# Kernel optimization log

Hardware: AMD Instinct MI355X
Metric: run time of the kernel (lower is better)

Reference implementation:

```python
import jax, jax.numpy as jnp
import numpy as np

B, C, H, W = 8, 512, 64, 64
R = 16
CQK = C // R  # 32


def setup_inputs() -> dict:
    key = jax.random.key(0)
    kx, kq, kk, kv = jax.random.split(key, 4)
    x = jax.random.normal(kx, (B, C, H, W), dtype=jnp.float32)
    # Conv1d with kernel_size=1, bias=False == matmul over channel dim
    Wq = jax.random.normal(kq, (CQK, C), dtype=jnp.float32) * (1.0 / np.sqrt(C))
    Wk = jax.random.normal(kk, (CQK, C), dtype=jnp.float32) * (1.0 / np.sqrt(C))
    Wv = jax.random.normal(kv, (C, C), dtype=jnp.float32) * (1.0 / np.sqrt(C))
    return {"x": x, "Wq": Wq, "Wk": Wk, "Wv": Wv}


def reference(x, Wq, Wk, Wv):
    b, c, h, w = x.shape
    xf = x.reshape(b, c, h * w)                 # [b, c, n]
    q = jnp.einsum('dc,bcn->bdn', Wq, xf)       # [b, c/r, n]
    k = jnp.einsum('dc,bcn->bdn', Wk, xf)       # [b, c/r, n]
    attn = jax.nn.softmax(jnp.einsum('bdm,bdn->bmn', q, k), axis=-1)  # [b, n, n]
    v = jnp.einsum('dc,bcn->bdn', Wv, xf)       # [b, c, n]
    out = jnp.einsum('bcm,bmn->bcn', v, attn)   # [b, c, n]
    return out.reshape(b, c, h, w)
```

## Files before the change

### kernel.cpp

```cpp
#include <hip/hip_runtime.h>
#include <hip/hip_bf16.h>


typedef __attribute__((ext_vector_type(8))) short s16x8;
typedef __attribute__((ext_vector_type(4))) float f32x4;

#define MFMA16(a, b, c) __builtin_amdgcn_mfma_f32_16x16x32_bf16((a), (b), (c), 0, 0, 0)

__device__ __forceinline__ ushort f2bf(float f) {
  union { float f; unsigned u; } v; v.f = f;
  return (ushort)((v.u + 0x8000u) >> 16);
}
__device__ __forceinline__ unsigned pack_bf16(float lo, float hi) {
  union { float f; unsigned u; } a, b; a.f = lo; b.f = hi;
  return __builtin_amdgcn_perm(b.u + 0x8000u, a.u + 0x8000u, 0x07060302u);
}
__device__ __forceinline__ float fexp2(float x) { return __builtin_amdgcn_exp2f(x); }

__device__ __forceinline__ void chunk_barrier() {
  asm volatile("s_waitcnt lgkmcnt(0)" ::: "memory");
  __builtin_amdgcn_s_barrier();
  __builtin_amdgcn_sched_barrier(0);
}

__global__ void k_cvt_w(const float* __restrict__ Wq, const float* __restrict__ Wk,
                        const float* __restrict__ Wv, ushort* __restrict__ Wqb,
                        ushort* __restrict__ Wkb, ushort* __restrict__ Wvb) {
  int i = blockIdx.x * 256 + threadIdx.x;
  if (i < 262144) Wvb[i] = f2bf(Wv[i]);
  else if (i < 278528) Wqb[i - 262144] = f2bf(Wq[i - 262144] * 1.4426950408889634f);
  else if (i < 294912) Wkb[i - 278528] = f2bf(Wk[i - 278528]);
}

__global__ __launch_bounds__(256, 2) void k_proj(const float* __restrict__ x,
                                                 const ushort* __restrict__ Wqb,
                                                 const ushort* __restrict__ Wkb,
                                                 const ushort* __restrict__ Wvb,
                                                 ushort* __restrict__ qb,
                                                 ushort* __restrict__ kb,
                                                 ushort* __restrict__ vb) {
  const int b = blockIdx.y, n0 = blockIdx.x * 64;
  const int t = threadIdx.x;
  const int lane = t & 63, w = t >> 6;
  const int quad = lane >> 4, l15 = lane & 15;

  __shared__ __align__(16) ushort XB[64 * 512];
  __shared__ uint U[2][32][17];

  const float* x_b = x + (size_t)b * 512 * 4096;

  for (int s = 0; s < 16; ++s) {
    const int c0s = s * 32;
#pragma unroll
    for (int k = 0; k < 2; ++k) {
      const int idx = t + k * 256;
      const int cr = idx >> 4, c4 = idx & 15;
      float4 f = *(const float4*)(x_b + (size_t)(c0s + cr) * 4096 + n0 + c4 * 4);
      U[0][cr][c4] = pack_bf16(f.x, f.y);
      U[1][cr][c4] = pack_bf16(f.z, f.w);
    }
    __syncthreads();
    {
      const int n = t & 63, gl = t >> 6;
      const int h = (n >> 1) & 1, c4 = n >> 2;
      const uint sel = (n & 1) ? 0x07060302u : 0x05040100u;
      uint o[4];
#pragma unroll
      for (int j = 0; j < 4; ++j) {
        uint ua = U[h][gl * 8 + 2 * j][c4];
        uint ub = U[h][gl * 8 + 2 * j + 1][c4];
        o[j] = __builtin_amdgcn_perm(ub, ua, sel);
      }
      const int gfull = (c0s >> 3) + gl;
      const int gsw = gfull ^ (n & 7);
      *(uint4*)((char*)XB + n * 1024 + gsw * 16) = *(uint4*)o;
    }
    __syncthreads();
  }

  const ushort* Wqk = (w < 2) ? (Wqb + (size_t)(w * 16 + l15) * 512)
                              : (Wkb + (size_t)((w - 2) * 16 + l15) * 512);

  f32x4 accv[8][4], accqk[4];
#pragma unroll
  for (int i = 0; i < 8; ++i)
#pragma unroll
    for (int nt = 0; nt < 4; ++nt) accv[i][nt] = {0.f, 0.f, 0.f, 0.f};
#pragma unroll
  for (int nt = 0; nt < 4; ++nt) accqk[nt] = {0.f, 0.f, 0.f, 0.f};

  const char* XBb = (const char*)XB;
  for (int k0 = 0; k0 < 512; k0 += 32) {
    s16x8 bx[4];
#pragma unroll
    for (int nt = 0; nt < 4; ++nt) {
      const int nl = nt * 16 + l15;
      bx[nt] = *(const s16x8*)(XBb + nl * 1024 + ((((k0 >> 3) + quad) ^ (nl & 7)) << 4));
    }
#pragma unroll
    for (int i = 0; i < 8; ++i) {
      s16x8 av = *(const s16x8*)(Wvb + (size_t)((8 * w + i) * 16 + l15) * 512 + k0 + quad * 8);
#pragma unroll
      for (int nt = 0; nt < 4; ++nt) accv[i][nt] = MFMA16(av, bx[nt], accv[i][nt]);
    }
    s16x8 aqk = *(const s16x8*)(Wqk + k0 + quad * 8);
#pragma unroll
    for (int nt = 0; nt < 4; ++nt) accqk[nt] = MFMA16(aqk, bx[nt], accqk[nt]);
  }

  ushort* vb_b = vb + (size_t)b * 512 * 4096;
#pragma unroll
  for (int i = 0; i < 8; ++i)
#pragma unroll
    for (int nt = 0; nt < 4; ++nt)
#pragma unroll
      for (int r = 0; r < 4; ++r)
        vb_b[(size_t)((8 * w + i) * 16 + quad * 4 + r) * 4096 + n0 + nt * 16 + l15] =
            f2bf(accv[i][nt][r]);

  ushort* qk_out = (w < 2) ? (qb + (size_t)b * 4096 * 32) : (kb + (size_t)b * 4096 * 32);
#pragma unroll
  for (int nt = 0; nt < 4; ++nt) {
    ushort4 u;
    u.x = f2bf(accqk[nt][0]); u.y = f2bf(accqk[nt][1]);
    u.z = f2bf(accqk[nt][2]); u.w = f2bf(accqk[nt][3]);
    *(ushort4*)(qk_out + (size_t)(n0 + nt * 16 + l15) * 32 + (w & 1) * 16 + quad * 4) = u;
  }
}

__global__ __launch_bounds__(256) void k_pass1(const ushort* __restrict__ qb,
                                               const ushort* __restrict__ kb,
                                               float* __restrict__ Lneg) {
  const int b = blockIdx.y, mt = blockIdx.x;
  const int lane = threadIdx.x & 63, w = threadIdx.x >> 6;
  const int quad = lane >> 4, l15 = lane & 15;
  const int m = mt * 64 + w * 16;
  const ushort* qb_b = qb + (size_t)b * 4096 * 32;
  const ushort* kb_b = kb + (size_t)b * 4096 * 32;
  const s16x8 aqf = *(const s16x8*)(qb_b + (size_t)(m + l15) * 32 + quad * 8);
  float ps[4] = {0.f, 0.f, 0.f, 0.f};
  const f32x4 zf = {0.f, 0.f, 0.f, 0.f};
  for (int n0 = 0; n0 < 4096; n0 += 64) {
#pragma unroll
    for (int nt = 0; nt < 4; ++nt) {
      s16x8 bk = *(const s16x8*)(kb_b + (size_t)(n0 + nt * 16 + l15) * 32 + quad * 8);
      f32x4 s = MFMA16(aqf, bk, zf);
#pragma unroll
      for (int r = 0; r < 4; ++r) ps[r] += fexp2(s[r]);
    }
  }
  for (int off = 1; off < 16; off <<= 1)
#pragma unroll
    for (int r = 0; r < 4; ++r) ps[r] += __shfl_xor(ps[r], off, 64);
  if (l15 == 0)
#pragma unroll
    for (int r = 0; r < 4; ++r)
      Lneg[(size_t)b * 4096 + m + quad * 4 + r] = -log2f(ps[r]);
}

__global__ __launch_bounds__(512, 2) void k_pass2(const ushort* __restrict__ qb,
                                                  const ushort* __restrict__ kb,
                                                  const ushort* __restrict__ vb,
                                                  const float* __restrict__ Lneg,
                                                  float* __restrict__ out) {
  const int blk = blockIdx.x;
  const int b = blk & 7, ntb = blk >> 3;
  const int nbase = ntb * 128;
  const int lane = threadIdx.x & 63, w = threadIdx.x >> 6;
  const int quad = lane >> 4, l15 = lane & 15;
  const int cbase = w * 64;
  const int swz = l15 & 7;
  const int Mw = w >> 1;
  const int Tb = (w & 1) * 4;

  __shared__ __align__(16) ushort PT[2][128 * 64];

  const ushort* qb_b = qb + (size_t)b * 4096 * 32;
  const ushort* kb_b = kb + (size_t)b * 4096 * 32;
  const ushort* vb_b = vb + (size_t)b * 512 * 4096;
  const float* L_b = Lneg + (size_t)b * 4096;

  s16x8 kf[4];
#pragma unroll
  for (int i = 0; i < 4; ++i)
    kf[i] = *(const s16x8*)(kb_b + (size_t)(nbase + (Tb + i) * 16 + l15) * 32 + quad * 8);

  f32x4 acc[4][8];
#pragma unroll
  for (int ci = 0; ci < 4; ++ci)
#pragma unroll
    for (int nt = 0; nt < 8; ++nt) acc[ci][nt] = {0.f, 0.f, 0.f, 0.f};

  s16x8 aqp;
  float4 l4p;
  s16x8 va0[4], va1[4];

  auto loadQ = [&](int chunk) {
    const int m0 = chunk * 64;
    aqp = *(const s16x8*)(qb_b + (size_t)(m0 + Mw * 16 + l15) * 32 + quad * 8);
    l4p = *(const float4*)(L_b + m0 + Mw * 16 + quad * 4);
  };
  auto loadV0 = [&](int chunk) {
    const int m0 = chunk * 64;
#pragma unroll
    for (int ci = 0; ci < 4; ++ci)
      va0[ci] = *(const s16x8*)(vb_b + (size_t)(cbase + ci * 16 + l15) * 4096 + m0 + quad * 8);
  };
  auto loadV1 = [&](int chunk) {
    const int m0 = chunk * 64;
#pragma unroll
    for (int ci = 0; ci < 4; ++ci)
      va1[ci] = *(const s16x8*)(vb_b + (size_t)(cbase + ci * 16 + l15) * 4096 + m0 + 32 + quad * 8);
  };
  auto produce_tile = [&](int buf, int i) {
    char* Pw = (char*)&PT[buf][0];
    const int T = Tb + i;
    f32x4 cin; cin.x = l4p.x; cin.y = l4p.y; cin.z = l4p.z; cin.w = l4p.w;
    f32x4 s = MFMA16(aqp, kf[i], cin);
    uint2 u;
    u.x = pack_bf16(fexp2(s.x), fexp2(s.y));
    u.y = pack_bf16(fexp2(s.z), fexp2(s.w));
    const int row = T * 16 + l15;
    const int gran = (2 * Mw + (quad >> 1)) ^ swz;
    *(uint2*)(Pw + row * 128 + gran * 16 + (quad & 1) * 8) = u;
  };

  loadQ(0);
#pragma unroll
  for (int i = 0; i < 4; ++i) produce_tile(0, i);
  loadQ(1);
  loadV0(0);
  loadV1(0);

  for (int chunk = 0; chunk < 64; ++chunk) {
    const int buf = chunk & 1;
    chunk_barrier();
    const char* P = (const char*)&PT[buf][0];
    s16x8 pg[8];
#pragma unroll
    for (int nt = 0; nt < 8; ++nt)
      pg[nt] = *(const s16x8*)(P + (nt * 16 + l15) * 128 + (quad ^ swz) * 16);
#pragma unroll
    for (int i = 0; i < 4; ++i) produce_tile(buf ^ 1, i);
    if (chunk < 62) loadQ(chunk + 2);
    __builtin_amdgcn_s_setprio(1);
    s16x8 rr[8];
#pragma unroll
    for (int nt = 0; nt < 8; ++nt) {
#pragma unroll
      for (int ci = 0; ci < 4; ++ci) acc[ci][nt] = MFMA16(va0[ci], pg[nt], acc[ci][nt]);
      rr[nt] = *(const s16x8*)(P + (nt * 16 + l15) * 128 + ((4 + quad) ^ swz) * 16);
    }
    __builtin_amdgcn_s_setprio(0);
    if (chunk < 63) loadV0(chunk + 1);
    __builtin_amdgcn_s_setprio(1);
#pragma unroll
    for (int nt = 0; nt < 8; ++nt)
#pragma unroll
      for (int ci = 0; ci < 4; ++ci) acc[ci][nt] = MFMA16(va1[ci], rr[nt], acc[ci][nt]);
    __builtin_amdgcn_s_setprio(0);
    if (chunk < 63) loadV1(chunk + 1);
  }

  float* out_b = out + (size_t)b * 512 * 4096;
#pragma unroll
  for (int ci = 0; ci < 4; ++ci)
#pragma unroll
    for (int nt = 0; nt < 8; ++nt) {
      const int n = nbase + nt * 16 + l15;
      const int c0 = cbase + ci * 16 + quad * 4;
#pragma unroll
      for (int r = 0; r < 4; ++r) out_b[(size_t)(c0 + r) * 4096 + n] = acc[ci][nt][r];
    }
}

extern "C" void kernel_launch(void* const* d_in, const int* in_sizes, int n_in,
                              void* d_out, int out_size, void* d_ws, size_t ws_size,
                              hipStream_t stream) {
  const float* x  = (const float*)d_in[0];
  const float* Wq = (const float*)d_in[1];
  const float* Wk = (const float*)d_in[2];
  const float* Wv = (const float*)d_in[3];
  float* out = (float*)d_out;

  char* ws = (char*)d_ws;
  ushort* vb  = (ushort*)(ws + 0);
  ushort* qb  = (ushort*)(ws + 33554432);
  ushort* kb  = (ushort*)(ws + 35651584);
  ushort* Wvb = (ushort*)(ws + 37748736);
  ushort* Wqb = (ushort*)(ws + 38273024);
  ushort* Wkb = (ushort*)(ws + 38305792);
  float*  Lrs = (float*)(ws + 38338560);

  hipLaunchKernelGGL(k_cvt_w, dim3(1152), dim3(256), 0, stream, Wq, Wk, Wv, Wqb, Wkb, Wvb);
  hipLaunchKernelGGL(k_proj, dim3(64, 8), dim3(256), 0, stream, x, Wqb, Wkb, Wvb, qb, kb, vb);
  hipLaunchKernelGGL(k_pass1, dim3(64, 8), dim3(256), 0, stream, qb, kb, Lrs);
  hipLaunchKernelGGL(k_pass2, dim3(256), dim3(512), 0, stream, qb, kb, vb, Lrs, out);
}
```

Measured before the change: 322.5 us.

## Double-buffer x staging in projection kernel and vectorize V output stores

The x-to-bf16 transpose staging in k_proj becomes a software pipeline with a double-buffered U scratch: the global loads for the next chunks are issued before the current chunk is packed and transposed, so load latency overlaps LDS work. Separately, the V MFMA operands are swapped so each lane's accumulator holds 4 consecutive n values, which lets the V output be written as ushort4 vector stores instead of scalar strided stores. This costs more registers and LDS for the second buffer, and the projection kernel is only one of several kernels in the pipeline.

```diff
diff --git a/kernel.cpp b/kernel.cpp
--- a/kernel.cpp
+++ b/kernel.cpp
@@ -45,35 +45,54 @@
   const int quad = lane >> 4, l15 = lane & 15;
 
   __shared__ __align__(16) ushort XB[64 * 512];
-  __shared__ uint U[2][32][17];
+  __shared__ uint U[2][2][32][17];
 
   const float* x_b = x + (size_t)b * 512 * 4096;
 
-  for (int s = 0; s < 16; ++s) {
+  auto ldX = [&](int s, float4& fa, float4& fb) {
     const int c0s = s * 32;
-#pragma unroll
-    for (int k = 0; k < 2; ++k) {
-      const int idx = t + k * 256;
-      const int cr = idx >> 4, c4 = idx & 15;
-      float4 f = *(const float4*)(x_b + (size_t)(c0s + cr) * 4096 + n0 + c4 * 4);
-      U[0][cr][c4] = pack_bf16(f.x, f.y);
-      U[1][cr][c4] = pack_bf16(f.z, f.w);
-    }
+    const float* p = x_b + (size_t)(c0s + (t >> 4)) * 4096 + n0 + (t & 15) * 4;
+    fa = *(const float4*)p;
+    fb = *(const float4*)(p + (size_t)16 * 4096);
+  };
+  auto packU = [&](int ub, const float4& fa, const float4& fb) {
+    const int cr = t >> 4, c4 = t & 15;
+    U[ub][0][cr][c4] = pack_bf16(fa.x, fa.y);
+    U[ub][1][cr][c4] = pack_bf16(fa.z, fa.w);
+    U[ub][0][cr + 16][c4] = pack_bf16(fb.x, fb.y);
+    U[ub][1][cr + 16][c4] = pack_bf16(fb.z, fb.w);
+  };
+  auto phase2 = [&](int ub, int s) {
+    const int n = t & 63, gl = t >> 6;
+    const int h = (n >> 1) & 1, c4 = n >> 2;
+    const uint sel = (n & 1) ? 0x07060302u : 0x05040100u;
+    uint o[4];
+#pragma unroll
+    for (int j = 0; j < 4; ++j) {
+      uint ua = U[ub][h][gl * 8 + 2 * j][c4];
+      uint ubv = U[ub][h][gl * 8 + 2 * j + 1][c4];
+      o[j] = __builtin_amdgcn_perm(ubv, ua, sel);
+    }
+    const int gfull = s * 4 + gl;
+    const int gsw = gfull ^ (n & 7);
+    *(uint4*)((char*)XB + n * 1024 + gsw * 16) = *(uint4*)o;
+  };
+
+  float4 fa0, fb0, fa1, fb1;
+  ldX(0, fa0, fb0);
+  packU(0, fa0, fb0);
+  ldX(1, fa1, fb1);
+  __syncthreads();
+#pragma unroll
+  for (int s = 0; s < 16; s += 2) {
+    phase2(0, s);
+    if (s < 14) ldX(s + 2, fa0, fb0);
+    packU(1, fa1, fb1);
     __syncthreads();
-    {
-      const int n = t & 63, gl = t >> 6;
-      const int h = (n >> 1) & 1, c4 = n >> 2;
-      const uint sel = (n & 1) ? 0x07060302u : 0x05040100u;
-      uint o[4];
-#pragma unroll
-      for (int j = 0; j < 4; ++j) {
-        uint ua = U[h][gl * 8 + 2 * j][c4];
-        uint ub = U[h][gl * 8 + 2 * j + 1][c4];
-        o[j] = __builtin_amdgcn_perm(ub, ua, sel);
-      }
-      const int gfull = (c0s >> 3) + gl;
-      const int gsw = gfull ^ (n & 7);
-      *(uint4*)((char*)XB + n * 1024 + gsw * 16) = *(uint4*)o;
+    phase2(1, s + 1);
+    if (s < 14) {
+      packU(0, fa0, fb0);
+      ldX(s + 3, fa1, fb1);
     }
     __syncthreads();
   }
@@ -101,7 +120,7 @@
     for (int i = 0; i < 8; ++i) {
       s16x8 av = *(const s16x8*)(Wvb + (size_t)((8 * w + i) * 16 + l15) * 512 + k0 + quad * 8);
 #pragma unroll
-      for (int nt = 0; nt < 4; ++nt) accv[i][nt] = MFMA16(av, bx[nt], accv[i][nt]);
+      for (int nt = 0; nt < 4; ++nt) accv[i][nt] = MFMA16(bx[nt], av, accv[i][nt]);
     }
     s16x8 aqk = *(const s16x8*)(Wqk + k0 + quad * 8);
 #pragma unroll
@@ -112,11 +131,12 @@
 #pragma unroll
   for (int i = 0; i < 8; ++i)
 #pragma unroll
-    for (int nt = 0; nt < 4; ++nt)
-#pragma unroll
-      for (int r = 0; r < 4; ++r)
-        vb_b[(size_t)((8 * w + i) * 16 + quad * 4 + r) * 4096 + n0 + nt * 16 + l15] =
-            f2bf(accv[i][nt][r]);
+    for (int nt = 0; nt < 4; ++nt) {
+      ushort4 u;
+      u.x = f2bf(accv[i][nt][0]); u.y = f2bf(accv[i][nt][1]);
+      u.z = f2bf(accv[i][nt][2]); u.w = f2bf(accv[i][nt][3]);
+      *(ushort4*)(vb_b + (size_t)((8 * w + i) * 16 + l15) * 4096 + n0 + nt * 16 + quad * 4) = u;
+    }
 
   ushort* qk_out = (w < 2) ? (qb + (size_t)b * 4096 * 32) : (kb + (size_t)b * 4096 * 32);
 #pragma unroll
```

After: 321.5 us. Within noise of the previous version (-0.3%).
